# Optimization experiments

Hardware: AMD Instinct MI355X
Metric: run time of the kernel (lower is better)

The kernel has to match this reference:

```python
import jax, jax.numpy as jnp
import numpy as np

B, N, NQ, D, H = 16, 1024, 1024, 512, 8
HD = D // H  # per-head kq dim and per-head v-output dim (64)


def setup_inputs() -> dict:
    key = jax.random.key(0)
    ks = jax.random.split(key, 7)
    s = 0.02  # small init like torch Linear default scale
    return {
        "x":   jax.random.normal(ks[0], (B, N, D), jnp.float32),
        "r":   jax.random.normal(ks[1], (B, N, D), jnp.float32),
        "x_q": jax.random.normal(ks[2], (B, NQ, D), jnp.float32),
        # per-head projection weights, torch Linear layout (out, in), stacked over heads
        "Wq": jax.random.normal(ks[3], (H, HD, D), jnp.float32) * s,
        "Wk": jax.random.normal(ks[4], (H, HD, D), jnp.float32) * s,
        "Wv": jax.random.normal(ks[5], (H, HD, D), jnp.float32) * s,  # applied AFTER attention
        "Wo": jax.random.normal(ks[6], (D, D), jnp.float32) * s,
    }


def reference(x, r, x_q, Wq, Wk, Wv, Wo):
    # AttentionAggregator.forward(x, r, x_q) -> MultiHeadAttention(q=x_q, k=x, v=r)
    qh = jnp.einsum('bnd,hed->bhne', x_q, Wq)            # (B,H,NQ,HD)
    kh = jnp.einsum('bmd,hed->bhme', x, Wk)              # (B,H,N,HD)
    scale = jnp.sqrt(jnp.float32(HD))                    # sqrt(d_k) with d_k = head_kq_dim_out
    scores = jnp.einsum('bhne,bhme->bhnm', qh, kh) / scale
    attn = jax.nn.softmax(scores, axis=-1)               # normalize=True path
    # NOTE: v (=r) is NOT projected before attention in the original module
    ctx = jnp.einsum('bhnm,bmd->bhnd', attn, r)          # (B,H,NQ,D)
    heads = jnp.einsum('bhnd,hed->bhne', ctx, Wv)        # (B,H,NQ,HD), per-head post-projection
    concat = heads.transpose(0, 2, 1, 3).reshape(B, NQ, H * HD)  # cat over heads, dim=-1
    return concat @ Wo.T                                 # head_o (post_process=True)
```

## Files before the change

### kernel.cpp

```cpp
#include <hip/hip_runtime.h>


#define B_  16
#define N_  1024
#define D_  512
#define M_  (B_ * N_)

typedef short short8 __attribute__((ext_vector_type(8)));
typedef float f32x4 __attribute__((ext_vector_type(4)));
typedef unsigned short ushort;
typedef unsigned int uint;

__device__ __forceinline__ ushort bf16rne(float f) {
  uint u = __float_as_uint(f);
  u += 0x7FFFu + ((u >> 16) & 1u);
  return (ushort)(u >> 16);
}
__device__ __forceinline__ uint bf16pk(float lo, float hi) {
  return (uint)bf16rne(lo) | ((uint)bf16rne(hi) << 16);
}
__device__ __forceinline__ void gload_lds16(const void* g, void* l) {
  __builtin_amdgcn_global_load_lds(
      (const __attribute__((address_space(1))) uint*)g,
      (__attribute__((address_space(3))) uint*)l, 16, 0, 0);
}
__device__ __forceinline__ float exp2_hw(float x) {
  float r;
  asm("v_exp_f32 %0, %1" : "=v"(r) : "v"(x));
  return r;
}
__device__ __forceinline__ uint cvtpk_bf16(float lo, float hi) {
  uint r;
  asm("v_cvt_pk_bf16_f32 %0, %1, %2" : "=v"(r) : "v"(lo), "v"(hi));
  return r;
}

union U4S8 { uint u[4]; short8 s; };

__global__ __launch_bounds__(256) void cast3_k(
    const float* __restrict__ s0, const float* __restrict__ s1,
    const float* __restrict__ s2, ushort* __restrict__ d, long n)
{
  const float* s = (blockIdx.y == 0) ? s0 : (blockIdx.y == 1) ? s1 : s2;
  ushort* dz = d + (long)blockIdx.y * n;
  long i = ((long)blockIdx.x * 256 + threadIdx.x) * 8;
  float4 v0 = *(const float4*)(s + i);
  float4 v1 = *(const float4*)(s + i + 4);
  uint4 o;
  o.x = bf16pk(v0.x, v0.y); o.y = bf16pk(v0.z, v0.w);
  o.z = bf16pk(v1.x, v1.y); o.w = bf16pk(v1.z, v1.w);
  *(uint4*)(dz + i) = o;
}

__global__ __launch_bounds__(256) void castW_k(
    const float* __restrict__ w0, const float* __restrict__ w1,
    const float* __restrict__ w2, const float* __restrict__ w3,
    ushort* __restrict__ d, long n)
{
  const int z = blockIdx.y;
  const float* s = (z == 0) ? w0 : (z == 1) ? w1 : (z == 2) ? w2 : w3;
  const float sc = (z == 0) ? 0.1803368801f : 1.f;
  ushort* dz = d + (long)z * n;
  long i = ((long)blockIdx.x * 256 + threadIdx.x) * 8;
  float4 v0 = *(const float4*)(s + i);
  float4 v1 = *(const float4*)(s + i + 4);
  uint4 o;
  o.x = bf16pk(v0.x * sc, v0.y * sc); o.y = bf16pk(v0.z * sc, v0.w * sc);
  o.z = bf16pk(v1.x * sc, v1.y * sc); o.w = bf16pk(v1.z * sc, v1.w * sc);
  *(uint4*)(dz + i) = o;
}

template <int MODE>
__global__ __launch_bounds__(256) void gemm_k(
    const ushort* __restrict__ Abase, const ushort* __restrict__ Wbase,
    void* __restrict__ C0, ushort* __restrict__ Vt)
{
  const long SB = (long)M_ * D_, WB = (long)D_ * D_;
  const int z = (MODE == 0) ? blockIdx.z : 0;
  const ushort* A = Abase + z * SB;
  const ushort* W = Wbase + z * WB;

  __shared__ __align__(16) ushort Al[128 * 64];
  __shared__ __align__(16) ushort Bl[128 * 64];
  const int t = threadIdx.x, lane = t & 63, w = t >> 6;
  const int g = lane >> 4, lr = lane & 15;
  const int wr = w >> 1, wc = w & 1;
  const long m0 = (long)blockIdx.y * 128, n0 = (long)blockIdx.x * 128;

  f32x4 acc[4][4] = {};

  for (int k0 = 0; k0 < D_; k0 += 64) {
    __syncthreads();
    #pragma unroll
    for (int u = 0; u < 4; ++u) {
      const int a = t * 16 + u * 4096;
      const int row = a >> 7, ch = (a >> 4) & 7;
      const int kk = k0 + ((ch ^ (row & 7)) << 3);
      gload_lds16(A + (m0 + row) * D_ + kk, (char*)Al + a);
      gload_lds16(W + (n0 + row) * D_ + kk, (char*)Bl + a);
    }
    __syncthreads();

    short8 af[4][2], bf[4][2];
    #pragma unroll
    for (int mf = 0; mf < 4; ++mf)
      #pragma unroll
      for (int ks = 0; ks < 2; ++ks) {
        int row = wr * 64 + mf * 16 + lr;
        af[mf][ks] = *(const short8*)((const char*)Al + row * 128 + (((ks * 4 + g) ^ (row & 7)) << 4));
        row = wc * 64 + mf * 16 + lr;
        bf[mf][ks] = *(const short8*)((const char*)Bl + row * 128 + (((ks * 4 + g) ^ (row & 7)) << 4));
      }
    #pragma unroll
    for (int mf = 0; mf < 4; ++mf)
      #pragma unroll
      for (int nf = 0; nf < 4; ++nf)
        #pragma unroll
        for (int ks = 0; ks < 2; ++ks)
          acc[mf][nf] = __builtin_amdgcn_mfma_f32_16x16x32_bf16(
              af[mf][ks], bf[nf][ks], acc[mf][nf], 0, 0, 0);
  }

  if constexpr (MODE == 1) {
    float* C = (float*)C0;
    #pragma unroll
    for (int mf = 0; mf < 4; ++mf)
      #pragma unroll
      for (int nf = 0; nf < 4; ++nf)
        #pragma unroll
        for (int r = 0; r < 4; ++r)
          C[(m0 + wr * 64 + mf * 16 + g * 4 + r) * D_ + n0 + wc * 64 + nf * 16 + lr] =
              acc[mf][nf][r];
  } else {
    if (z < 2) {
      ushort* C = (ushort*)C0 + z * SB;
      #pragma unroll
      for (int mf = 0; mf < 4; ++mf)
        #pragma unroll
        for (int nf = 0; nf < 4; ++nf)
          #pragma unroll
          for (int r = 0; r < 4; ++r)
            C[(m0 + wr * 64 + mf * 16 + g * 4 + r) * D_ + n0 + wc * 64 + nf * 16 + lr] =
                bf16rne(acc[mf][nf][r]);
    } else {
      const int hh = (int)(n0 >> 6) + wc;
      #pragma unroll
      for (int mf = 0; mf < 4; ++mf) {
        const long m = m0 + wr * 64 + mf * 16 + g * 4;
        const int bb = (int)(m >> 10);
        const int kv = (int)(m & 1023);
        #pragma unroll
        for (int nf = 0; nf < 4; ++nf) {
          const int c = nf * 16 + lr;
          ushort4 o4;
          o4.x = bf16rne(acc[mf][nf][0]); o4.y = bf16rne(acc[mf][nf][1]);
          o4.z = bf16rne(acc[mf][nf][2]); o4.w = bf16rne(acc[mf][nf][3]);
          *(ushort4*)&Vt[((long)(bb * 8 + hh) * 64 + c) * (long)N_ + kv] = o4;
        }
      }
    }
  }
}

__global__ __launch_bounds__(256) void attn_mfma(
    const ushort* __restrict__ Q, const ushort* __restrict__ K,
    const ushort* __restrict__ Vt, ushort* __restrict__ Hd)
{
  __shared__ __align__(16) ushort Kl[2][64 * 64];
  __shared__ __align__(16) ushort Vl[2][64 * 64];
  const int t = threadIdx.x, lane = t & 63, w = t >> 6;
  const int g = lane >> 4, lr = lane & 15;
  const int bid = blockIdx.x;
  const int z = bid & 127, b = z >> 3, h = z & 7;
  const int qbase = (bid >> 7) * 128 + w * 32;

  short8 qf[2][2];
  #pragma unroll
  for (int nf = 0; nf < 2; ++nf)
    #pragma unroll
    for (int ks = 0; ks < 2; ++ks)
      qf[nf][ks] = *(const short8*)(Q + (long)(b * N_ + qbase + nf * 16 + lr) * D_ + h * 64 + ks * 32 + g * 8);

  f32x4 o[2][4] = {};
  float lsum[2] = {0.f, 0.f};

  const ushort* Kz = K + (long)b * N_ * D_ + h * 64;
  const ushort* Vz = Vt + (long)z * 64 * N_;

  auto STAGE = [&](int kt, int bufi) {
    #pragma unroll
    for (int u = 0; u < 2; ++u) {
      const int a = t * 16 + u * 4096;
      const int row = a >> 7, ch = (a >> 4) & 7;
      const int cc = (ch ^ (row & 7)) << 3;
      gload_lds16(Kz + (long)(kt * 64 + row) * D_ + cc, (char*)Kl[bufi] + a);
      gload_lds16(Vz + (long)row * N_ + kt * 64 + cc, (char*)Vl[bufi] + a);
    }
  };

  STAGE(0, 0);
  __syncthreads();

  for (int kt = 0; kt < 16; ++kt) {
    const int cur = kt & 1;
    if (kt < 15) STAGE(kt + 1, cur ^ 1);

    f32x4 s[4][2] = {};
    #pragma unroll
    for (int mf = 0; mf < 4; ++mf) {
      short8 kf[2];
      #pragma unroll
      for (int ks = 0; ks < 2; ++ks) {
        const int row = mf * 16 + lr;
        kf[ks] = *(const short8*)((const char*)Kl[cur] + row * 128 + (((ks * 4 + g) ^ (row & 7)) << 4));
      }
      #pragma unroll
      for (int nf = 0; nf < 2; ++nf)
        #pragma unroll
        for (int ks = 0; ks < 2; ++ks)
          s[mf][nf] = __builtin_amdgcn_mfma_f32_16x16x32_bf16(kf[ks], qf[nf][ks], s[mf][nf], 0, 0, 0);
    }

    short8 pa[2][2];
    #pragma unroll
    for (int nf = 0; nf < 2; ++nf) {
      uint Apk[4], Bpk[4];
      #pragma unroll
      for (int mf = 0; mf < 4; ++mf) {
        const float e0 = exp2_hw(s[mf][nf][0]);
        const float e1 = exp2_hw(s[mf][nf][1]);
        const float e2 = exp2_hw(s[mf][nf][2]);
        const float e3 = exp2_hw(s[mf][nf][3]);
        lsum[nf] += (e0 + e1) + (e2 + e3);
        Apk[mf] = cvtpk_bf16(e0, e1);
        Bpk[mf] = cvtpk_bf16(e2, e3);
      }
      asm("v_permlane32_swap_b32 %0, %1" : "+v"(Apk[0]), "+v"(Apk[1]));
      asm("v_permlane16_swap_b32 %0, %1" : "+v"(Apk[0]), "+v"(Apk[1]));
      asm("v_permlane32_swap_b32 %0, %1" : "+v"(Bpk[0]), "+v"(Bpk[1]));
      asm("v_permlane16_swap_b32 %0, %1" : "+v"(Bpk[0]), "+v"(Bpk[1]));
      asm("v_permlane32_swap_b32 %0, %1" : "+v"(Apk[2]), "+v"(Apk[3]));
      asm("v_permlane16_swap_b32 %0, %1" : "+v"(Apk[2]), "+v"(Apk[3]));
      asm("v_permlane32_swap_b32 %0, %1" : "+v"(Bpk[2]), "+v"(Bpk[3]));
      asm("v_permlane16_swap_b32 %0, %1" : "+v"(Bpk[2]), "+v"(Bpk[3]));
      U4S8 u0, u1;
      u0.u[0] = Apk[0]; u0.u[1] = Bpk[0]; u0.u[2] = Apk[1]; u0.u[3] = Bpk[1];
      u1.u[0] = Apk[2]; u1.u[1] = Bpk[2]; u1.u[2] = Apk[3]; u1.u[3] = Bpk[3];
      pa[nf][0] = u0.s;
      pa[nf][1] = u1.s;
    }

    #pragma unroll
    for (int ks = 0; ks < 2; ++ks) {
      short8 vb[4];
      #pragma unroll
      for (int nf = 0; nf < 4; ++nf) {
        const int row = nf * 16 + lr;
        vb[nf] = *(const short8*)((const char*)Vl[cur] + row * 128 + (((ks * 4 + g) ^ (row & 7)) << 4));
      }
      #pragma unroll
      for (int mf = 0; mf < 2; ++mf)
        #pragma unroll
        for (int nf = 0; nf < 4; ++nf)
          o[mf][nf] = __builtin_amdgcn_mfma_f32_16x16x32_bf16(pa[mf][ks], vb[nf], o[mf][nf], 0, 0, 0);
    }
    __syncthreads();
  }

  #pragma unroll
  for (int nf = 0; nf < 2; ++nf) {
    lsum[nf] += __shfl_xor(lsum[nf], 16);
    lsum[nf] += __shfl_xor(lsum[nf], 32);
  }

  #pragma unroll
  for (int mf = 0; mf < 2; ++mf)
    #pragma unroll
    for (int r = 0; r < 4; ++r) {
      const float inv = 1.f / __shfl(lsum[mf], g * 4 + r);
      const long grow = (long)b * N_ + qbase + mf * 16 + g * 4 + r;
      #pragma unroll
      for (int nf = 0; nf < 4; ++nf)
        Hd[grow * D_ + h * 64 + nf * 16 + lr] = bf16rne(o[mf][nf][r] * inv);
    }
}

extern "C" void kernel_launch(void* const* d_in, const int* in_sizes, int n_in,
                              void* d_out, int out_size, void* d_ws, size_t ws_size,
                              hipStream_t stream) {
  const float* x   = (const float*)d_in[0];
  const float* r   = (const float*)d_in[1];
  const float* x_q = (const float*)d_in[2];
  const float* Wq  = (const float*)d_in[3];
  const float* Wk  = (const float*)d_in[4];
  const float* Wv  = (const float*)d_in[5];
  const float* Wo  = (const float*)d_in[6];

  const long SBe = (long)M_ * D_;
  const long WBe = (long)D_ * D_;
  ushort* xqb = (ushort*)d_ws;
  ushort* xb  = xqb + SBe;
  ushort* rb  = xb  + SBe;
  ushort* Qb  = rb  + SBe;
  ushort* Kb  = Qb  + SBe;
  ushort* Vtb = Kb  + SBe;
  ushort* Wqb = Vtb + SBe;
  ushort* Hdb = xqb;

  dim3 blk(256);
  cast3_k<<<dim3(4096, 3), blk, 0, stream>>>(x_q, x, r, xqb, SBe);
  castW_k<<<dim3(128, 4),  blk, 0, stream>>>(Wq, Wk, Wv, Wo, Wqb, WBe);

  gemm_k<0><<<dim3(4, 128, 3), blk, 0, stream>>>(xqb, Wqb, Qb, Vtb);

  attn_mfma<<<dim3(1024), blk, 0, stream>>>(Qb, Kb, Vtb, Hdb);

  gemm_k<1><<<dim3(4, 128), blk, 0, stream>>>(Hdb, Wqb + 3 * WBe, d_out, nullptr);
}
```

Before: 269.1 us.

## Double-buffer GEMM LDS staging and remap workgroups across XCDs

Replaces the single-buffered GEMM k-loop with a two-stage LDS pipeline: the next tiles are issued via global_load_lds while MFMAs run on the current buffer, with vmcnt waits controlling completion. It also flattens the grid to 1D and remaps block IDs so consecutive tiles sharing A rows land on the same XCD, aiming for better L2 reuse. LDS use doubles to 64KB per block, which may reduce occupancy. This touches only the projection and output GEMMs; attention is unchanged.

```diff
diff --git a/kernel.cpp b/kernel.cpp
--- a/kernel.cpp
+++ b/kernel.cpp
@@ -76,30 +76,43 @@
     void* __restrict__ C0, ushort* __restrict__ Vt)
 {
   const long SB = (long)M_ * D_, WB = (long)D_ * D_;
-  const int z = (MODE == 0) ? blockIdx.z : 0;
+  const int nwg = gridDim.x, per = nwg >> 3;
+  const int wg = ((int)blockIdx.x & 7) * per + ((int)blockIdx.x >> 3);
+  int z, bx, by;
+  if constexpr (MODE == 0) { z = wg >> 9; bx = wg & 3; by = (wg & 511) >> 2; }
+  else                     { z = 0;       bx = wg & 3; by = wg >> 2; }
   const ushort* A = Abase + z * SB;
   const ushort* W = Wbase + z * WB;
 
-  __shared__ __align__(16) ushort Al[128 * 64];
-  __shared__ __align__(16) ushort Bl[128 * 64];
+  __shared__ __align__(16) ushort Al[2][128 * 64];
+  __shared__ __align__(16) ushort Bl[2][128 * 64];
   const int t = threadIdx.x, lane = t & 63, w = t >> 6;
   const int g = lane >> 4, lr = lane & 15;
   const int wr = w >> 1, wc = w & 1;
-  const long m0 = (long)blockIdx.y * 128, n0 = (long)blockIdx.x * 128;
+  const long m0 = (long)by * 128, n0 = (long)bx * 128;
 
   f32x4 acc[4][4] = {};
 
-  for (int k0 = 0; k0 < D_; k0 += 64) {
-    __syncthreads();
+  auto STAGE = [&](int k0, int bufi) {
     #pragma unroll
     for (int u = 0; u < 4; ++u) {
       const int a = t * 16 + u * 4096;
       const int row = a >> 7, ch = (a >> 4) & 7;
       const int kk = k0 + ((ch ^ (row & 7)) << 3);
-      gload_lds16(A + (m0 + row) * D_ + kk, (char*)Al + a);
-      gload_lds16(W + (n0 + row) * D_ + kk, (char*)Bl + a);
-    }
-    __syncthreads();
+      gload_lds16(A + (m0 + row) * D_ + kk, (char*)Al[bufi] + a);
+      gload_lds16(W + (n0 + row) * D_ + kk, (char*)Bl[bufi] + a);
+    }
+  };
+
+  STAGE(0, 0);
+  STAGE(64, 1);
+
+  #pragma unroll
+  for (int it = 0; it < 8; ++it) {
+    const int cur = it & 1;
+    if (it < 7) asm volatile("s_waitcnt vmcnt(8)" ::: "memory");
+    else        asm volatile("s_waitcnt vmcnt(0)" ::: "memory");
+    __builtin_amdgcn_s_barrier();
 
     short8 af[4][2], bf[4][2];
     #pragma unroll
@@ -107,9 +120,9 @@
       #pragma unroll
       for (int ks = 0; ks < 2; ++ks) {
         int row = wr * 64 + mf * 16 + lr;
-        af[mf][ks] = *(const short8*)((const char*)Al + row * 128 + (((ks * 4 + g) ^ (row & 7)) << 4));
+        af[mf][ks] = *(const short8*)((const char*)Al[cur] + row * 128 + (((ks * 4 + g) ^ (row & 7)) << 4));
         row = wc * 64 + mf * 16 + lr;
-        bf[mf][ks] = *(const short8*)((const char*)Bl + row * 128 + (((ks * 4 + g) ^ (row & 7)) << 4));
+        bf[mf][ks] = *(const short8*)((const char*)Bl[cur] + row * 128 + (((ks * 4 + g) ^ (row & 7)) << 4));
       }
     #pragma unroll
     for (int mf = 0; mf < 4; ++mf)
@@ -119,6 +132,10 @@
         for (int ks = 0; ks < 2; ++ks)
           acc[mf][nf] = __builtin_amdgcn_mfma_f32_16x16x32_bf16(
               af[mf][ks], bf[nf][ks], acc[mf][nf], 0, 0, 0);
+
+    asm volatile("s_waitcnt lgkmcnt(0)" ::: "memory");
+    __builtin_amdgcn_s_barrier();
+    if (it < 6) STAGE((it + 2) * 64, cur);
   }
 
   if constexpr (MODE == 1) {
@@ -311,9 +328,9 @@
   cast3_k<<<dim3(4096, 3), blk, 0, stream>>>(x_q, x, r, xqb, SBe);
   castW_k<<<dim3(128, 4),  blk, 0, stream>>>(Wq, Wk, Wv, Wo, Wqb, WBe);
 
-  gemm_k<0><<<dim3(4, 128, 3), blk, 0, stream>>>(xqb, Wqb, Qb, Vtb);
+  gemm_k<0><<<dim3(1536), blk, 0, stream>>>(xqb, Wqb, Qb, Vtb);
 
   attn_mfma<<<dim3(1024), blk, 0, stream>>>(Qb, Kb, Vtb, Hdb);
 
-  gemm_k<1><<<dim3(4, 128), blk, 0, stream>>>(Hdb, Wqb + 3 * WBe, d_out, nullptr);
-}
+  gemm_k<1><<<dim3(512), blk, 0, stream>>>(Hdb, Wqb + 3 * WBe, d_out, nullptr);
+}
```

Result: faster. 245.7 us (-8.7%).
